# Optimization experiments

Measured on AMD Instinct MI355X. Metric: run time of the kernel, lower is better.

## Reference

```python
import jax, jax.numpy as jnp
import numpy as np

N, W, D, IC, OC, R = 256, 1, 64, 32, 32, 8


def setup_inputs() -> dict:
    key = jax.random.key(0)
    k1, k2 = jax.random.split(key)
    x = jax.random.normal(k1, (N, W, D, IC, R), dtype=jnp.float32)
    weights = jax.random.normal(k2, (D, IC, OC, R), dtype=jnp.float32)
    return {"x": x, "weights": weights}


def reference(x, weights):
    # x: [n, w, d, ic, r] -> [n, w, d, ic, 1, r]
    # weights: [d, ic, oc, r] -> broadcast as [1, 1, d, ic, oc, r]
    # out: logsumexp over ic -> [n, w, d, oc, r]
    logits = x[:, :, :, :, None, :] + weights[None, None]
    return jax.nn.logsumexp(logits, axis=3)
```

## Files before the change

kernel.cpp:

```cpp
#include <hip/hip_runtime.h>


constexpr int kN = 256, kD = 64, kIC = 32, kOC = 32, kR = 8;
constexpr int kNT = 32;
constexpr int PAD = 36;
constexpr int PQ  = PAD / 4;

__global__ __launch_bounds__(256) void lse_kernel(
    const float* __restrict__ x, const float* __restrict__ w,
    float* __restrict__ out)
{
    __shared__ __align__(16) float ws[kIC * kR * PAD];
    __shared__ __align__(16) float xs[kNT * kR * PAD];

    const int t  = threadIdx.x;
    const int d  = blockIdx.x;
    const int n0 = blockIdx.y * kNT;

    {
        const float4* wg = reinterpret_cast<const float4*>(w + (size_t)d * (kIC * kOC * kR));
        #pragma unroll
        for (int i = 0; i < 8; ++i) {
            const int qg = i * 256 + t;
            float4 v = wg[qg];
            const int lin = qg * 4;
            const int ic = lin >> 8;
            const int oc = (lin >> 3) & 31;
            const int r0 = lin & 7;
            const int j  = (oc & 3) * 8 + (oc >> 2);
            float* p = &ws[(ic * kR + r0) * PAD + j];
            p[0 * PAD] = __expf(v.x);
            p[1 * PAD] = __expf(v.y);
            p[2 * PAD] = __expf(v.z);
            p[3 * PAD] = __expf(v.w);
        }
    }

    {
        #pragma unroll
        for (int i = 0; i < 8; ++i) {
            const int fidx = i * 256 + t;
            const int nl = fidx >> 6;
            const int e  = fidx & 63;
            const float4* xg = reinterpret_cast<const float4*>(
                x + (size_t)(n0 + nl) * (kD * kIC * kR) + (size_t)d * (kIC * kR));
            float4 v = xg[e];
            const int ic = e >> 1;
            const int r0 = (e & 1) * 4;
            float* p = &xs[(nl * kR + r0) * PAD + ic];
            p[0 * PAD] = __expf(v.x);
            p[1 * PAD] = __expf(v.y);
            p[2 * PAD] = __expf(v.z);
            p[3 * PAD] = __expf(v.w);
        }
    }

    __syncthreads();

    const int rr  = t & 7;
    const int och = (t >> 3) & 3;
    const int ng  = t >> 5;

    float acc[4][8];
    #pragma unroll
    for (int jj = 0; jj < 4; ++jj)
        #pragma unroll
        for (int k = 0; k < 8; ++k)
            acc[jj][k] = 0.f;

    const float4* xs4 = reinterpret_cast<const float4*>(xs);
    const float4* ws4 = reinterpret_cast<const float4*>(ws);

    #pragma unroll
    for (int icq = 0; icq < 8; ++icq) {
        float4 xv[4];
        #pragma unroll
        for (int jj = 0; jj < 4; ++jj)
            xv[jj] = xs4[((ng * 4 + jj) * kR + rr) * PQ + icq];
        #pragma unroll
        for (int q = 0; q < 4; ++q) {
            const int ic = icq * 4 + q;
            const float4 w0 = ws4[(ic * kR + rr) * PQ + och * 2];
            const float4 w1 = ws4[(ic * kR + rr) * PQ + och * 2 + 1];
            #pragma unroll
            for (int jj = 0; jj < 4; ++jj) {
                const float* xp = reinterpret_cast<const float*>(&xv[jj]);
                const float xq = xp[q];
                acc[jj][0] = fmaf(xq, w0.x, acc[jj][0]);
                acc[jj][1] = fmaf(xq, w0.y, acc[jj][1]);
                acc[jj][2] = fmaf(xq, w0.z, acc[jj][2]);
                acc[jj][3] = fmaf(xq, w0.w, acc[jj][3]);
                acc[jj][4] = fmaf(xq, w1.x, acc[jj][4]);
                acc[jj][5] = fmaf(xq, w1.y, acc[jj][5]);
                acc[jj][6] = fmaf(xq, w1.z, acc[jj][6]);
                acc[jj][7] = fmaf(xq, w1.w, acc[jj][7]);
            }
        }
    }

    #pragma unroll
    for (int jj = 0; jj < 4; ++jj) {
        const int n = n0 + ng * 4 + jj;
        float* op = out + (size_t)n * (kD * kOC * kR) + (size_t)d * (kOC * kR)
                    + och * 8 + rr;
        #pragma unroll
        for (int k = 0; k < 8; ++k)
            op[k * 32] = __logf(acc[jj][k]);
    }
}

extern "C" void kernel_launch(void* const* d_in, const int* in_sizes, int n_in,
                              void* d_out, int out_size, void* d_ws, size_t ws_size,
                              hipStream_t stream) {
    const float* x = (const float*)d_in[0];
    const float* w = (const float*)d_in[1];
    float* out = (float*)d_out;
    dim3 grid(kD, kN / kNT);
    lse_kernel<<<grid, 256, 0, stream>>>(x, w, out);
}
```

Measured before the change: 15.03 us.

## Double n-tile per block, prefetch second x chunk during first compute

Each block now covers 64 n instead of 32, so the exp of the weight tile is computed once per 64 n rather than once per 32. The second half of x is loaded into registers before the first compute, so that load can overlap with the math. The thread mapping changes to 8 n by 4 oc per thread with a reworked LDS weight layout. The grid halves to 256 blocks on a GPU with 256 CUs and LDS usage grows, so parallelism and occupancy may drop.

Result: slower. 17.74 us (+18.1%).

```diff
diff --git a/kernel.cpp b/kernel.cpp
--- a/kernel.cpp
+++ b/kernel.cpp
@@ -1,112 +1,148 @@
 #include <hip/hip_runtime.h>
 
 
-constexpr int kN = 256, kD = 64, kIC = 32, kOC = 32, kR = 8;
-constexpr int kNT = 32;
-constexpr int PAD = 36;
-constexpr int PQ  = PAD / 4;
+constexpr int kD = 64, kIC = 32, kOC = 32, kR = 8;
+constexpr int kNT = 64;
+constexpr int PAD = 36, PQ = PAD / 4;
+constexpr int WS_FLOATS = kIC * kR * PAD;
+constexpr int XS_FLOATS = kNT * kR * PAD;
+constexpr size_t LDS_BYTES = (size_t)(WS_FLOATS + XS_FLOATS) * 4;
 
-__global__ __launch_bounds__(256) void lse_kernel(
-    const float* __restrict__ x, const float* __restrict__ w,
-    float* __restrict__ out)
+__device__ __forceinline__ void compute_store_chunk(
+    const float* __restrict__ xs, const float* __restrict__ ws,
+    float* __restrict__ out, int t, int d, int n0, int cbase)
 {
-    __shared__ __align__(16) float ws[kIC * kR * PAD];
-    __shared__ __align__(16) float xs[kNT * kR * PAD];
+    const int rr  = t & 7;
+    const int och = (t >> 3) & 7;
+    const int ng  = t >> 6;
+    const int nbase = cbase + ng * 8;
 
-    const int t  = threadIdx.x;
-    const int d  = blockIdx.x;
-    const int n0 = blockIdx.y * kNT;
-
-    {
-        const float4* wg = reinterpret_cast<const float4*>(w + (size_t)d * (kIC * kOC * kR));
+    float acc[8][4];
+    #pragma unroll
+    for (int jj = 0; jj < 8; ++jj)
         #pragma unroll
-        for (int i = 0; i < 8; ++i) {
-            const int qg = i * 256 + t;
-            float4 v = wg[qg];
-            const int lin = qg * 4;
-            const int ic = lin >> 8;
-            const int oc = (lin >> 3) & 31;
-            const int r0 = lin & 7;
-            const int j  = (oc & 3) * 8 + (oc >> 2);
-            float* p = &ws[(ic * kR + r0) * PAD + j];
-            p[0 * PAD] = __expf(v.x);
-            p[1 * PAD] = __expf(v.y);
-            p[2 * PAD] = __expf(v.z);
-            p[3 * PAD] = __expf(v.w);
-        }
-    }
-
-    {
-        #pragma unroll
-        for (int i = 0; i < 8; ++i) {
-            const int fidx = i * 256 + t;
-            const int nl = fidx >> 6;
-            const int e  = fidx & 63;
-            const float4* xg = reinterpret_cast<const float4*>(
-                x + (size_t)(n0 + nl) * (kD * kIC * kR) + (size_t)d * (kIC * kR));
-            float4 v = xg[e];
-            const int ic = e >> 1;
-            const int r0 = (e & 1) * 4;
-            float* p = &xs[(nl * kR + r0) * PAD + ic];
-            p[0 * PAD] = __expf(v.x);
-            p[1 * PAD] = __expf(v.y);
-            p[2 * PAD] = __expf(v.z);
-            p[3 * PAD] = __expf(v.w);
-        }
-    }
-
-    __syncthreads();
-
-    const int rr  = t & 7;
-    const int och = (t >> 3) & 3;
-    const int ng  = t >> 5;
-
-    float acc[4][8];
-    #pragma unroll
-    for (int jj = 0; jj < 4; ++jj)
-        #pragma unroll
-        for (int k = 0; k < 8; ++k)
-            acc[jj][k] = 0.f;
+        for (int k = 0; k < 4; ++k) acc[jj][k] = 0.f;
 
     const float4* xs4 = reinterpret_cast<const float4*>(xs);
     const float4* ws4 = reinterpret_cast<const float4*>(ws);
 
     #pragma unroll
     for (int icq = 0; icq < 8; ++icq) {
-        float4 xv[4];
+        float4 xq[8];
         #pragma unroll
-        for (int jj = 0; jj < 4; ++jj)
-            xv[jj] = xs4[((ng * 4 + jj) * kR + rr) * PQ + icq];
+        for (int jj = 0; jj < 8; ++jj)
+            xq[jj] = xs4[((nbase + jj) * kR + rr) * PQ + icq];
         #pragma unroll
         for (int q = 0; q < 4; ++q) {
-            const int ic = icq * 4 + q;
-            const float4 w0 = ws4[(ic * kR + rr) * PQ + och * 2];
-            const float4 w1 = ws4[(ic * kR + rr) * PQ + och * 2 + 1];
+            const float4 wq = ws4[((icq * 4 + q) * kR + rr) * PQ + och];
             #pragma unroll
-            for (int jj = 0; jj < 4; ++jj) {
-                const float* xp = reinterpret_cast<const float*>(&xv[jj]);
-                const float xq = xp[q];
-                acc[jj][0] = fmaf(xq, w0.x, acc[jj][0]);
-                acc[jj][1] = fmaf(xq, w0.y, acc[jj][1]);
-                acc[jj][2] = fmaf(xq, w0.z, acc[jj][2]);
-                acc[jj][3] = fmaf(xq, w0.w, acc[jj][3]);
-                acc[jj][4] = fmaf(xq, w1.x, acc[jj][4]);
-                acc[jj][5] = fmaf(xq, w1.y, acc[jj][5]);
-                acc[jj][6] = fmaf(xq, w1.z, acc[jj][6]);
-                acc[jj][7] = fmaf(xq, w1.w, acc[jj][7]);
+            for (int jj = 0; jj < 8; ++jj) {
+                const float xqq = reinterpret_cast<const float*>(&xq[jj])[q];
+                acc[jj][0] = fmaf(xqq, wq.x, acc[jj][0]);
+                acc[jj][1] = fmaf(xqq, wq.y, acc[jj][1]);
+                acc[jj][2] = fmaf(xqq, wq.z, acc[jj][2]);
+                acc[jj][3] = fmaf(xqq, wq.w, acc[jj][3]);
             }
         }
     }
 
     #pragma unroll
-    for (int jj = 0; jj < 4; ++jj) {
-        const int n = n0 + ng * 4 + jj;
+    for (int jj = 0; jj < 8; ++jj) {
+        const int n = n0 + nbase + jj;
         float* op = out + (size_t)n * (kD * kOC * kR) + (size_t)d * (kOC * kR)
                     + och * 8 + rr;
         #pragma unroll
-        for (int k = 0; k < 8; ++k)
-            op[k * 32] = __logf(acc[jj][k]);
+        for (int k = 0; k < 4; ++k)
+            op[k * 64] = __logf(acc[jj][k]);
     }
+}
+
+__global__ __launch_bounds__(256, 1) void lse_kernel(
+    const float* __restrict__ x, const float* __restrict__ w,
+    float* __restrict__ out)
+{
+    extern __shared__ float lds[];
+    float* ws = lds;
+    float* xs = lds + WS_FLOATS;
+
+    const int t  = threadIdx.x;
+    const int d  = blockIdx.x;
+    const int n0 = blockIdx.y * kNT;
+
+    const float4* wg = reinterpret_cast<const float4*>(w + (size_t)d * (kIC * kOC * kR));
+    float4 wv[8];
+    #pragma unroll
+    for (int i = 0; i < 8; ++i) wv[i] = wg[i * 256 + t];
+
+    float4 x0v[8];
+    #pragma unroll
+    for (int i = 0; i < 8; ++i) {
+        const int fidx = i * 256 + t;
+        const int nl = fidx >> 6;
+        const int e  = fidx & 63;
+        x0v[i] = reinterpret_cast<const float4*>(
+            x + (size_t)(n0 + nl) * (kD * kIC * kR) + (size_t)d * (kIC * kR))[e];
+    }
+
+    #pragma unroll
+    for (int i = 0; i < 8; ++i) {
+        const int lin = (i * 256 + t) * 4;
+        const int ic = lin >> 8;
+        const int oc = (lin >> 3) & 31;
+        const int r0 = lin & 7;
+        const int j  = (oc & 7) * 4 + (oc >> 3);
+        float* p = &ws[(ic * kR + r0) * PAD + j];
+        p[0 * PAD] = __expf(wv[i].x);
+        p[1 * PAD] = __expf(wv[i].y);
+        p[2 * PAD] = __expf(wv[i].z);
+        p[3 * PAD] = __expf(wv[i].w);
+    }
+
+    #pragma unroll
+    for (int i = 0; i < 8; ++i) {
+        const int fidx = i * 256 + t;
+        const int nl = fidx >> 6;
+        const int e  = fidx & 63;
+        const int ic = e >> 1;
+        const int r0 = (e & 1) * 4;
+        float* p = &xs[(nl * kR + r0) * PAD + ic];
+        p[0 * PAD] = __expf(x0v[i].x);
+        p[1 * PAD] = __expf(x0v[i].y);
+        p[2 * PAD] = __expf(x0v[i].z);
+        p[3 * PAD] = __expf(x0v[i].w);
+    }
+
+    float4 x1v[8];
+    #pragma unroll
+    for (int i = 0; i < 8; ++i) {
+        const int fidx = i * 256 + t;
+        const int nl = fidx >> 6;
+        const int e  = fidx & 63;
+        x1v[i] = reinterpret_cast<const float4*>(
+            x + (size_t)(n0 + 32 + nl) * (kD * kIC * kR) + (size_t)d * (kIC * kR))[e];
+    }
+
+    __syncthreads();
+
+    compute_store_chunk(xs, ws, out, t, d, n0, 0);
+
+    #pragma unroll
+    for (int i = 0; i < 8; ++i) {
+        const int fidx = i * 256 + t;
+        const int nl = fidx >> 6;
+        const int e  = fidx & 63;
+        const int ic = e >> 1;
+        const int r0 = (e & 1) * 4;
+        float* p = &xs[((32 + nl) * kR + r0) * PAD + ic];
+        p[0 * PAD] = __expf(x1v[i].x);
+        p[1 * PAD] = __expf(x1v[i].y);
+        p[2 * PAD] = __expf(x1v[i].z);
+        p[3 * PAD] = __expf(x1v[i].w);
+    }
+
+    __syncthreads();
+
+    compute_store_chunk(xs, ws, out, t, d, n0, 32);
 }
 
 extern "C" void kernel_launch(void* const* d_in, const int* in_sizes, int n_in,
@@ -115,6 +151,9 @@
     const float* x = (const float*)d_in[0];
     const float* w = (const float*)d_in[1];
     float* out = (float*)d_out;
-    dim3 grid(kD, kN / kNT);
-    lse_kernel<<<grid, 256, 0, stream>>>(x, w, out);
+    (void)hipFuncSetAttribute((const void*)lse_kernel,
+                              hipFuncAttributeMaxDynamicSharedMemorySize,
+                              (int)LDS_BYTES);
+    dim3 grid(kD, 256 / kNT);
+    lse_kernel<<<grid, 256, LDS_BYTES, stream>>>(x, w, out);
 }
```
